# Kernel optimization log

Measured on AMD Instinct MI355X. Metric: run time of the kernel, lower is better.

Reference implementation:

```python
import jax, jax.numpy as jnp
import numpy as np

IN_CH = 32
OUT_CH = 32
M1, M2 = 32, 32
BS, H, W = 8, 256, 256


def setup_inputs() -> dict:
    key = jax.random.key(0)
    kx, kk = jax.random.split(key)
    x = jax.random.normal(kx, (BS, IN_CH, H, W), dtype=jnp.float32)
    # reset_parameters: randn * (1/(in_ch*out_ch)) + 1
    scale = 1.0 / (IN_CH * OUT_CH)
    kernel = jax.random.normal(kk, (2, 1, OUT_CH, M1, M2, 2), dtype=jnp.float32) * scale + 1.0
    r = jnp.float32(1.0)
    return {"x": x, "kernel": kernel, "r": r}


def reference(x, kernel, r):
    # view_as_complex: last dim of 2 -> complex, shape [2, 1, C, M1, M2]
    kc = (kernel[..., 0] + 1j * kernel[..., 1]).astype(jnp.complex64)
    # elementwise complex power kernel**r
    kc = jnp.power(kc, r)

    # forward 2D real FFT over spatial dims (ortho norm)
    x_ft = jnp.fft.rfftn(x, axes=(-2, -1), norm="ortho")  # [bs, C, H, W//2+1]
    Hf, Wr = x_ft.shape[-2], x_ft.shape[-1]
    n1 = min(Hf // 2, M1)
    n2 = min(Wr, M2)

    def mix(block, k):
        # fft over channel dim (-3), multiply by complex kernel, ifft back
        b = jnp.fft.fft(block, axis=-3, norm="ortho")
        b = b * k[..., :n1, :n2]
        return jnp.fft.ifft(b, axis=-3, norm="ortho")

    pos = mix(x_ft[..., :n1, :n2], kc[0])          # low positive freqs
    neg = mix(x_ft[..., Hf - n1:, :n2], kc[1])     # low negative freqs

    out_ft = jnp.zeros((x.shape[0], OUT_CH, Hf, Wr), dtype=jnp.complex64)
    out_ft = out_ft.at[..., :n1, :n2].set(pos)
    out_ft = out_ft.at[..., Hf - n1:, :n2].set(neg)

    # inverse real FFT back to spatial domain
    return jnp.fft.irfftn(out_ft, s=(x.shape[-2], x.shape[-1]), axes=(-2, -1), norm="ortho")
```

## Files before the change

### kernel.cpp

```cpp
#include <hip/hip_runtime.h>
#include <math.h>


#define TWO_PI 6.28318530717958647692f

__global__ __launch_bounds__(256) void kP(const float* __restrict__ kin,
                                          const float* __restrict__ rp,
                                          float2* __restrict__ kp) {
  const int i = blockIdx.x * 256 + threadIdx.x;
  const float r = rp[0];
  const float kr = kin[2 * i], ki = kin[2 * i + 1];
  const float m2 = fmaf(kr, kr, ki * ki);
  float2 o = make_float2(0.f, 0.f);
  if (m2 > 0.f) {
    const float lm = 0.5f * logf(m2);
    const float ang = atan2f(ki, kr);
    const float mag = expf(r * lm);
    float s, c;
    sincosf(r * ang, &s, &c);
    o = make_float2(mag * c, mag * s);
  }
  kp[i] = o;
}

__global__ __launch_bounds__(256) void kA(const float* __restrict__ x,
                                          float2* __restrict__ z1) {
  __shared__ float xs[8192];
  const int tid = threadIdx.x;
  const long row0 = (long)blockIdx.x * 32;
  const float* xg = x + row0 * 256;
  {
    const int xl = tid & 31, rq = tid >> 5;
    const float* xgr = xg + rq * 4 * 256 + xl;
#pragma unroll
    for (int cb = 0; cb < 8; ++cb) {
      const int xc = xl + 32 * cb;
      const float4 v = make_float4(xgr[32 * cb], xgr[32 * cb + 256],
                                   xgr[32 * cb + 512], xgr[32 * cb + 768]);
      *(float4*)(xs + xc * 32 + 4 * ((rq + xc) & 7)) = v;
    }
  }
  __syncthreads();
  for (int i = tid; i < 127 * 32; i += 256) {
    const int xi = 1 + (i >> 5), r = i & 31;
    const int ai = (xi << 5) + ((r + 4 * xi) & 31);
    const int bi = ((256 - xi) << 5) + ((r - 4 * xi) & 31);
    const float a = xs[ai], b = xs[bi];
    xs[ai] = a + b;
    xs[bi] = a - b;
  }
  __syncthreads();
  const int w = tid & 31;
  const int r0 = (tid >> 5) << 2;
  int uo[8];
#pragma unroll
  for (int j = 0; j < 8; ++j) uo[j] = ((r0 + 4 * j) & 31) << 2;
  const float sgn = (w & 1) ? -1.f : 1.f;
  const float4 x0 = *(const float4*)(xs + r0);
  const float4 x128 = *(const float4*)(xs + (128 << 5) + r0);
  float Cr0 = fmaf(sgn, x128.x, x0.x), Cr1 = fmaf(sgn, x128.y, x0.y);
  float Cr2 = fmaf(sgn, x128.z, x0.z), Cr3 = fmaf(sgn, x128.w, x0.w);
  float Ci0 = 0, Ci1 = 0, Ci2 = 0, Ci3 = 0;
  float s1, c1;
  sincosf(TWO_PI * (float)w / 256.0f, &s1, &c1);
  float pc = c1, ps = s1;
  const char* const xsb = (const char*)xs;
#define KA_BODY(UPTR, VPTR)                                        \
  {                                                                \
    const float4 u = *(const float4*)(UPTR);                       \
    const float4 v = *(const float4*)(VPTR);                       \
    Cr0 = fmaf(u.x, pc, Cr0); Ci0 = fmaf(-v.x, ps, Ci0);           \
    Cr1 = fmaf(u.y, pc, Cr1); Ci1 = fmaf(-v.y, ps, Ci1);           \
    Cr2 = fmaf(u.z, pc, Cr2); Ci2 = fmaf(-v.z, ps, Ci2);           \
    Cr3 = fmaf(u.w, pc, Cr3); Ci3 = fmaf(-v.w, ps, Ci3);           \
    const float tn = fmaf(pc, c1, -ps * s1);                       \
    ps = fmaf(pc, s1, ps * c1);                                    \
    pc = tn;                                                       \
  }
  {
    const char* ub = xsb;
    const char* vb = xsb + 249 * 128;
#pragma unroll
    for (int j = 1; j < 8; ++j)
      KA_BODY(ub + j * 128 + uo[j], vb + (7 - j) * 128 + uo[8 - j])
  }
  for (int xb = 8; xb <= 120; xb += 8) {
    const char* ub = xsb + xb * 128;
    const char* vb = xsb + (249 - xb) * 128;
#pragma unroll
    for (int j = 0; j < 8; ++j)
      KA_BODY(ub + j * 128 + uo[j], vb + (7 - j) * 128 + uo[(8 - j) & 7])
  }
#undef KA_BODY
  float2* o = z1 + (row0 + r0) * 32 + w;
  o[0]  = make_float2(Cr0, Ci0);
  o[32] = make_float2(Cr1, Ci1);
  o[64] = make_float2(Cr2, Ci2);
  o[96] = make_float2(Cr3, Ci3);
}

__global__ __launch_bounds__(256) void kB1(float2* __restrict__ z1) {
  const int gt = blockIdx.x * 256 + threadIdx.x;
  const int w = gt & 31, y1 = (gt >> 5) & 31, bc = gt >> 10;
  float2* base = z1 + (long)bc * 8192 + y1 * 32 + w;
  float2 a[8];
#pragma unroll
  for (int j = 0; j < 8; ++j) a[j] = base[j * 1024];
  float2 t0 = make_float2(a[0].x + a[4].x, a[0].y + a[4].y);
  float2 t1 = make_float2(a[0].x - a[4].x, a[0].y - a[4].y);
  float2 t2 = make_float2(a[2].x + a[6].x, a[2].y + a[6].y);
  float2 t3 = make_float2(a[2].x - a[6].x, a[2].y - a[6].y);
  const float2 E0 = make_float2(t0.x + t2.x, t0.y + t2.y);
  const float2 E2 = make_float2(t0.x - t2.x, t0.y - t2.y);
  const float2 E1 = make_float2(t1.x + t3.y, t1.y - t3.x);
  const float2 E3 = make_float2(t1.x - t3.y, t1.y + t3.x);
  t0 = make_float2(a[1].x + a[5].x, a[1].y + a[5].y);
  t1 = make_float2(a[1].x - a[5].x, a[1].y - a[5].y);
  t2 = make_float2(a[3].x + a[7].x, a[3].y + a[7].y);
  t3 = make_float2(a[3].x - a[7].x, a[3].y - a[7].y);
  const float2 O0 = make_float2(t0.x + t2.x, t0.y + t2.y);
  const float2 O2 = make_float2(t0.x - t2.x, t0.y - t2.y);
  const float2 O1 = make_float2(t1.x + t3.y, t1.y - t3.x);
  const float2 O3 = make_float2(t1.x - t3.y, t1.y + t3.x);
  const float RT = 0.70710678118654752440f;
  const float2 B0 = O0;
  const float2 B1 = make_float2(RT * (O1.x + O1.y), RT * (O1.y - O1.x));
  const float2 B2 = make_float2(O2.y, -O2.x);
  const float2 B3 = make_float2(RT * (O3.y - O3.x), -RT * (O3.x + O3.y));
  base[0]        = make_float2(E0.x + B0.x, E0.y + B0.y);
  base[1 * 1024] = make_float2(E1.x + B1.x, E1.y + B1.y);
  base[2 * 1024] = make_float2(E2.x + B2.x, E2.y + B2.y);
  base[3 * 1024] = make_float2(E3.x + B3.x, E3.y + B3.y);
  base[4 * 1024] = make_float2(E0.x - B0.x, E0.y - B0.y);
  base[5 * 1024] = make_float2(E1.x - B1.x, E1.y - B1.y);
  base[6 * 1024] = make_float2(E2.x - B2.x, E2.y - B2.y);
  base[7 * 1024] = make_float2(E3.x - B3.x, E3.y - B3.y);
}

__global__ __launch_bounds__(256) void kB2(const float2* __restrict__ s,
                                           float2* __restrict__ z2) {
  const int bc = blockIdx.x >> 3, tq = blockIdx.x & 7;
  const int k = threadIdx.x >> 5, w = threadIdx.x & 31;
  const int t = tq * 8 + k;
  const int h = (t < 32) ? t : (192 + t);
  float sr, cr;
  sincosf(-TWO_PI * (float)h / 256.0f, &sr, &cr);
  const float2* src = s + (long)bc * 8192 + k * 1024 + w;
  float ar = 0.f, ai = 0.f;
  float pc = 1.f, ps = 0.f;
  for (int y1 = 0; y1 < 32; ++y1) {
    const float2 v = src[y1 * 32];
    ar = fmaf(v.x, pc, fmaf(-v.y, ps, ar));
    ai = fmaf(v.x, ps, fmaf( v.y, pc, ai));
    const float tn = fmaf(pc, cr, -ps * sr);
    ps = fmaf(pc, sr, ps * cr);
    pc = tn;
  }
  z2[(long)bc * 2048 + t * 32 + w] = make_float2(ar, ai);
}

__global__ __launch_bounds__(256) void kC(const float2* __restrict__ z2,
                                          const float2* __restrict__ kp,
                                          float2* __restrict__ g) {
  __shared__ float2 z2s[16 * 33];
  __shared__ float2 fk[16 * 33];
  __shared__ float2 tw[32];
  const int tid = threadIdx.x;
  if (tid < 32) {
    float s, c;
    sincosf(-TWO_PI * (float)tid / 32.0f, &s, &c);
    tw[tid] = make_float2(c, s);
  }
  const int m0 = blockIdx.x * 16;
  const int b = m0 >> 11;
  const int twi = m0 & 2047;
  const int t = twi >> 5;
  const int w0 = twi & 31;
  const int s_ = t >> 5, tm = t & 31;
  for (int i = tid; i < 512; i += 256) {
    const int ci = i >> 4, wj = i & 15;
    const long idx = ((long)(b * 32 + ci)) * 2048 + t * 32 + w0 + wj;
    z2s[wj * 33 + ci] = z2[idx];
  }
  __syncthreads();
  const int m = tid & 15;
  const int p = tid >> 4;
  const int cf0 = 2 * p, cf1 = 2 * p + 1;
  {
    float f0r = 0, f0i = 0, f1r = 0, f1i = 0;
    int i0 = 0, i1 = 0;
#pragma unroll 8
    for (int ci = 0; ci < 32; ++ci) {
      const float2 z = z2s[m * 33 + ci];
      const float2 t0 = tw[i0]; i0 = (i0 + cf0) & 31;
      const float2 t1 = tw[i1]; i1 = (i1 + cf1) & 31;
      f0r = fmaf(z.x, t0.x, fmaf(-z.y, t0.y, f0r));
      f0i = fmaf(z.x, t0.y, fmaf( z.y, t0.x, f0i));
      f1r = fmaf(z.x, t1.x, fmaf(-z.y, t1.y, f1r));
      f1i = fmaf(z.x, t1.y, fmaf( z.y, t1.x, f1i));
    }
    const float2 k0 = kp[((s_ * 32 + cf0) * 32 + tm) * 32 + w0 + m];
    const float2 k1 = kp[((s_ * 32 + cf1) * 32 + tm) * 32 + w0 + m];
    fk[m * 33 + cf0] = make_float2(f0r * k0.x - f0i * k0.y, f0r * k0.y + f0i * k0.x);
    fk[m * 33 + cf1] = make_float2(f1r * k1.x - f1i * k1.y, f1r * k1.y + f1i * k1.x);
  }
  __syncthreads();
  {
    float g0r = 0, g0i = 0, g1r = 0, g1i = 0;
    int i0 = 0, i1 = 0;
    const int co0 = 2 * p, co1 = 2 * p + 1;
#pragma unroll 8
    for (int cf = 0; cf < 32; ++cf) {
      const float2 f = fk[m * 33 + cf];
      const float2 t0 = tw[i0]; i0 = (i0 + co0) & 31;
      const float2 t1 = tw[i1]; i1 = (i1 + co1) & 31;
      g0r = fmaf(f.x, t0.x, fmaf( f.y, t0.y, g0r));
      g0i = fmaf(f.y, t0.x, fmaf(-f.x, t0.y, g0i));
      g1r = fmaf(f.x, t1.x, fmaf( f.y, t1.y, g1r));
      g1i = fmaf(f.y, t1.x, fmaf(-f.x, t1.y, g1i));
    }
    const float SC = 1.0f / 8192.0f;
    g[((long)(b * 32 + co0)) * 2048 + t * 32 + w0 + m] = make_float2(g0r * SC, g0i * SC);
    g[((long)(b * 32 + co1)) * 2048 + t * 32 + w0 + m] = make_float2(g1r * SC, g1i * SC);
  }
}

__global__ __launch_bounds__(256) void kD1(const float2* __restrict__ g,
                                           float2* __restrict__ U) {
  const int bc = blockIdx.x >> 3, y1q = blockIdx.x & 7;
  const int p = threadIdx.x >> 5, w = threadIdx.x & 31;
  const float2* gb = g + (long)bc * 2048 + w;
  float2* ub = U + (long)bc * 8192 + p * 32 + w;
#pragma unroll
  for (int y1l = 0; y1l < 4; ++y1l) {
    const int y1 = y1q * 4 + y1l;
    float st, ct;
    sincosf(TWO_PI * (float)y1 / 32.0f, &st, &ct);
    float s1, c1;
    sincosf(TWO_PI * (float)((p * y1) & 255) / 256.0f, &s1, &c1);
    float s2, c2;
    sincosf(TWO_PI * (float)(((224 + p) * y1) & 255) / 256.0f, &s2, &c2);
    float ar = 0.f, ai = 0.f;
    float pc = c1, ps = s1, qc = c2, qs = s2;
#pragma unroll
    for (int j = 0; j < 4; ++j) {
      const float2 va = gb[(p + 8 * j) * 32];
      const float2 vb = gb[(32 + p + 8 * j) * 32];
      ar = fmaf(va.x, pc, fmaf(-va.y, ps, ar));
      ai = fmaf(va.x, ps, fmaf( va.y, pc, ai));
      ar = fmaf(vb.x, qc, fmaf(-vb.y, qs, ar));
      ai = fmaf(vb.x, qs, fmaf( vb.y, qc, ai));
      const float tn = fmaf(pc, ct, -ps * st);
      ps = fmaf(pc, st, ps * ct);
      pc = tn;
      const float tm = fmaf(qc, ct, -qs * st);
      qs = fmaf(qc, st, qs * ct);
      qc = tm;
    }
    ub[y1 * 256] = make_float2(ar, ai);
  }
}

__global__ __launch_bounds__(256) void kDE(const float2* __restrict__ U,
                                           float* __restrict__ out) {
  __shared__ float2 tst[32 * 34];
  const int tid = threadIdx.x;
  const int bc = blockIdx.x >> 3, yq = blockIdx.x & 7;
  {
    const int y5 = tid >> 3, wq = tid & 7;
    const float* ub = (const float*)(U + (long)bc * 8192 + (long)y5 * 256 + wq * 4);
    float Tr[4] = {0.f, 0.f, 0.f, 0.f}, Ti[4] = {0.f, 0.f, 0.f, 0.f};
#pragma unroll
    for (int p = 0; p < 8; ++p) {
      float sp, cp;
      sincosf(TWO_PI * (float)((p * yq) & 7) / 8.0f, &sp, &cp);
      const float4 qa = *(const float4*)(ub + p * 64);
      const float4 qb = *(const float4*)(ub + p * 64 + 4);
      Tr[0] = fmaf(qa.x, cp, fmaf(-qa.y, sp, Tr[0]));
      Ti[0] = fmaf(qa.x, sp, fmaf( qa.y, cp, Ti[0]));
      Tr[1] = fmaf(qa.z, cp, fmaf(-qa.w, sp, Tr[1]));
      Ti[1] = fmaf(qa.z, sp, fmaf( qa.w, cp, Ti[1]));
      Tr[2] = fmaf(qb.x, cp, fmaf(-qb.y, sp, Tr[2]));
      Ti[2] = fmaf(qb.x, sp, fmaf( qb.y, cp, Ti[2]));
      Tr[3] = fmaf(qb.z, cp, fmaf(-qb.w, sp, Tr[3]));
      Ti[3] = fmaf(qb.z, sp, fmaf( qb.w, cp, Ti[3]));
    }
#pragma unroll
    for (int kk = 0; kk < 4; ++kk) {
      const int w = wq * 4 + kk;
      const float sc = w ? (2.0f / 256.0f) : (1.0f / 256.0f);
      tst[w * 34 + y5] = make_float2(Tr[kk] * sc, Ti[kk] * sc);
    }
  }
  __syncthreads();
  {
    const int xq = tid & 31;
    const int rh = tid >> 5;
    float sb, cb;
    sincosf(TWO_PI * (float)xq / 256.0f, &sb, &cb);
    const float RT = 0.70710678118654752440f;
    const float stc1 = RT * (cb - sb), sts1 = RT * (cb + sb);
    const float stc[4] = {cb, stc1, -sb, -sts1};
    const float sts[4] = {sb, sts1, cb, stc1};
    float C[4][4], S[4][4];
#pragma unroll
    for (int m = 0; m < 4; ++m)
#pragma unroll
      for (int j = 0; j < 4; ++j) { C[m][j] = 0.f; S[m][j] = 0.f; }
    float pc[4] = {1.f, 1.f, 1.f, 1.f}, ps[4] = {0.f, 0.f, 0.f, 0.f};
    const float* tbse = (const float*)tst + rh * 8;
#pragma unroll 2
    for (int w = 0; w < 32; ++w) {
      const float4 q0 = *(const float4*)(tbse + w * 68);
      const float4 q1 = *(const float4*)(tbse + w * 68 + 4);
#pragma unroll
      for (int m = 0; m < 4; ++m) {
        C[m][0] = fmaf(q0.x, pc[m], C[m][0]);
        S[m][0] = fmaf(q0.y, ps[m], S[m][0]);
        C[m][1] = fmaf(q0.z, pc[m], C[m][1]);
        S[m][1] = fmaf(q0.w, ps[m], S[m][1]);
        C[m][2] = fmaf(q1.x, pc[m], C[m][2]);
        S[m][2] = fmaf(q1.y, ps[m], S[m][2]);
        C[m][3] = fmaf(q1.z, pc[m], C[m][3]);
        S[m][3] = fmaf(q1.w, ps[m], S[m][3]);
        const float tn = fmaf(pc[m], stc[m], -ps[m] * sts[m]);
        ps[m] = fmaf(pc[m], sts[m], ps[m] * stc[m]);
        pc[m] = tn;
      }
    }
    const long rbase = (long)bc * 256 + yq * 32;
#pragma unroll
    for (int m = 0; m < 4; ++m) {
      const int xx = xq + 32 * m;
#pragma unroll
      for (int j = 0; j < 4; ++j) {
        const long row = rbase + rh * 4 + j;
        out[row * 256 + xx] = C[m][j] - S[m][j];
        out[row * 256 + ((256 - xx) & 255)] = C[m][j] + S[m][j];
      }
    }
    if (tid < 32) {
      float ae = 0.f, ao = 0.f;
#pragma unroll
      for (int k = 0; k < 16; ++k) {
        ae += tst[(2 * k) * 34 + tid].x;
        ao += tst[(2 * k + 1) * 34 + tid].x;
      }
      out[(rbase + tid) * 256 + 128] = ae - ao;
    }
  }
}

extern "C" void kernel_launch(void* const* d_in, const int* in_sizes, int n_in,
                              void* d_out, int out_size, void* d_ws, size_t ws_size,
                              hipStream_t stream) {
  const float* x = (const float*)d_in[0];
  const float* kin = (const float*)d_in[1];
  const float* rp = (const float*)d_in[2];
  float* out = (float*)d_out;
  char* ws = (char*)d_ws;

  float2* z1 = (float2*)(ws);
  float2* z2 = (float2*)(ws + (16ull << 20));
  float2* kp = (float2*)(ws + (24ull << 20));
  float2* g  = (float2*)(ws);
  float2* U  = (float2*)(ws + (4ull << 20));

  kP<<<256, 256, 0, stream>>>(kin, rp, kp);
  kA<<<2048, 256, 0, stream>>>(x, z1);
  kB1<<<1024, 256, 0, stream>>>(z1);
  kB2<<<2048, 256, 0, stream>>>(z1, z2);
  kC<<<1024, 256, 0, stream>>>(z2, kp, g);
  kD1<<<2048, 256, 0, stream>>>(g, U);
  kDE<<<2048, 256, 0, stream>>>(U, out);
}
```

Before: 217.0 us.

## Replace kA real-DFT folding with radix-8 butterfly and halve kC tile per block

```diff
diff --git a/kernel.cpp b/kernel.cpp
--- a/kernel.cpp
+++ b/kernel.cpp
@@ -41,57 +41,73 @@
     }
   }
   __syncthreads();
-  for (int i = tid; i < 127 * 32; i += 256) {
-    const int xi = 1 + (i >> 5), r = i & 31;
-    const int ai = (xi << 5) + ((r + 4 * xi) & 31);
-    const int bi = ((256 - xi) << 5) + ((r - 4 * xi) & 31);
-    const float a = xs[ai], b = xs[bi];
-    xs[ai] = a + b;
-    xs[bi] = a - b;
+  const float RT = 0.70710678118654752440f;
+#pragma unroll
+  for (int k = 0; k < 4; ++k) {
+    const int i = tid + (k << 8);
+    const int x1 = i >> 5, r = i & 31;
+    float* base = xs + x1 * 32 + ((r + 4 * x1) & 31);
+    const float a0 = base[0],        a1 = base[1024],     a2 = base[2048];
+    const float a3 = base[3 * 1024], a4 = base[4 * 1024], a5 = base[5 * 1024];
+    const float a6 = base[6 * 1024], a7 = base[7 * 1024];
+    const float t0 = a0 + a4, t1 = a0 - a4, t2 = a2 + a6, t3 = a2 - a6;
+    const float u0 = a1 + a5, u1 = a1 - a5, u2 = a3 + a7, u3 = a3 - a7;
+    const float E0 = t0 + t2, O0 = u0 + u2;
+    const float d1 = RT * (u1 - u3), d2 = RT * (u1 + u3);
+    base[0]        = E0 + O0;
+    base[1024]     = E0 - O0;
+    base[2 * 1024] = t1 + d1;
+    base[3 * 1024] = -(t3 + d2);
+    base[4 * 1024] = t0 - t2;
+    base[5 * 1024] = -(u0 - u2);
+    base[6 * 1024] = t1 - d1;
+    base[7 * 1024] = t3 - d2;
   }
   __syncthreads();
   const int w = tid & 31;
   const int r0 = (tid >> 5) << 2;
-  int uo[8];
-#pragma unroll
-  for (int j = 0; j < 8; ++j) uo[j] = ((r0 + 4 * j) & 31) << 2;
-  const float sgn = (w & 1) ? -1.f : 1.f;
-  const float4 x0 = *(const float4*)(xs + r0);
-  const float4 x128 = *(const float4*)(xs + (128 << 5) + r0);
-  float Cr0 = fmaf(sgn, x128.x, x0.x), Cr1 = fmaf(sgn, x128.y, x0.y);
-  float Cr2 = fmaf(sgn, x128.z, x0.z), Cr3 = fmaf(sgn, x128.w, x0.w);
+  const int p = w & 7;
+  int pr, pi;
+  float si;
+  if (p == 0)      { pr = 0;           pi = 0;      si = 0.f; }
+  else if (p == 4) { pr = 1;           pi = 1;      si = 0.f; }
+  else if (p < 4)  { pr = 2 * p;       pi = pr + 1; si = 1.f; }
+  else             { pr = 2 * (8 - p); pi = pr + 1; si = -1.f; }
+  const char* ur = (const char*)xs + pr * 4096;
+  const char* ui = (const char*)xs + pi * 4096;
+  const char* urp[8];
+  const char* uip[8];
+#pragma unroll
+  for (int j = 0; j < 8; ++j) {
+    const int off = 4 * ((r0 + 4 * j) & 31) + 128 * j;
+    urp[j] = ur + off;
+    uip[j] = ui + off;
+  }
+  float s1, c1;
+  sincosf(-TWO_PI * (float)w / 256.0f, &s1, &c1);
+  float pc = 1.f, ps = 0.f;
+  float Cr0 = 0, Cr1 = 0, Cr2 = 0, Cr3 = 0;
   float Ci0 = 0, Ci1 = 0, Ci2 = 0, Ci3 = 0;
-  float s1, c1;
-  sincosf(TWO_PI * (float)w / 256.0f, &s1, &c1);
-  float pc = c1, ps = s1;
-  const char* const xsb = (const char*)xs;
-#define KA_BODY(UPTR, VPTR)                                        \
-  {                                                                \
-    const float4 u = *(const float4*)(UPTR);                       \
-    const float4 v = *(const float4*)(VPTR);                       \
-    Cr0 = fmaf(u.x, pc, Cr0); Ci0 = fmaf(-v.x, ps, Ci0);           \
-    Cr1 = fmaf(u.y, pc, Cr1); Ci1 = fmaf(-v.y, ps, Ci1);           \
-    Cr2 = fmaf(u.z, pc, Cr2); Ci2 = fmaf(-v.z, ps, Ci2);           \
-    Cr3 = fmaf(u.w, pc, Cr3); Ci3 = fmaf(-v.w, ps, Ci3);           \
-    const float tn = fmaf(pc, c1, -ps * s1);                       \
-    ps = fmaf(pc, s1, ps * c1);                                    \
-    pc = tn;                                                       \
-  }
-  {
-    const char* ub = xsb;
-    const char* vb = xsb + 249 * 128;
-#pragma unroll
-    for (int j = 1; j < 8; ++j)
-      KA_BODY(ub + j * 128 + uo[j], vb + (7 - j) * 128 + uo[8 - j])
-  }
-  for (int xb = 8; xb <= 120; xb += 8) {
-    const char* ub = xsb + xb * 128;
-    const char* vb = xsb + (249 - xb) * 128;
-#pragma unroll
-    for (int j = 0; j < 8; ++j)
-      KA_BODY(ub + j * 128 + uo[j], vb + (7 - j) * 128 + uo[(8 - j) & 7])
-  }
-#undef KA_BODY
+#pragma unroll
+  for (int bq = 0; bq < 4; ++bq) {
+#pragma unroll
+    for (int j = 0; j < 8; ++j) {
+      const float4 Fr = *(const float4*)(urp[j] + bq * 1024);
+      const float4 Fi = *(const float4*)(uip[j] + bq * 1024);
+      const float qs = si * ps, qc = si * pc;
+      Cr0 = fmaf(Fr.x, pc, fmaf(-Fi.x, qs, Cr0));
+      Ci0 = fmaf(Fr.x, ps, fmaf( Fi.x, qc, Ci0));
+      Cr1 = fmaf(Fr.y, pc, fmaf(-Fi.y, qs, Cr1));
+      Ci1 = fmaf(Fr.y, ps, fmaf( Fi.y, qc, Ci1));
+      Cr2 = fmaf(Fr.z, pc, fmaf(-Fi.z, qs, Cr2));
+      Ci2 = fmaf(Fr.z, ps, fmaf( Fi.z, qc, Ci2));
+      Cr3 = fmaf(Fr.w, pc, fmaf(-Fi.w, qs, Cr3));
+      Ci3 = fmaf(Fr.w, ps, fmaf( Fi.w, qc, Ci3));
+      const float tn = fmaf(pc, c1, -ps * s1);
+      ps = fmaf(pc, s1, ps * c1);
+      pc = tn;
+    }
+  }
   float2* o = z1 + (row0 + r0) * 32 + w;
   o[0]  = make_float2(Cr0, Ci0);
   o[32] = make_float2(Cr1, Ci1);
@@ -162,8 +178,8 @@
 __global__ __launch_bounds__(256) void kC(const float2* __restrict__ z2,
                                           const float2* __restrict__ kp,
                                           float2* __restrict__ g) {
-  __shared__ float2 z2s[16 * 33];
-  __shared__ float2 fk[16 * 33];
+  __shared__ float2 z2s[8 * 33];
+  __shared__ float2 fk[8 * 33];
   __shared__ float2 tw[32];
   const int tid = threadIdx.x;
   if (tid < 32) {
@@ -171,57 +187,46 @@
     sincosf(-TWO_PI * (float)tid / 32.0f, &s, &c);
     tw[tid] = make_float2(c, s);
   }
-  const int m0 = blockIdx.x * 16;
+  const int m0 = blockIdx.x * 8;
   const int b = m0 >> 11;
   const int twi = m0 & 2047;
   const int t = twi >> 5;
   const int w0 = twi & 31;
   const int s_ = t >> 5, tm = t & 31;
-  for (int i = tid; i < 512; i += 256) {
-    const int ci = i >> 4, wj = i & 15;
-    const long idx = ((long)(b * 32 + ci)) * 2048 + t * 32 + w0 + wj;
-    z2s[wj * 33 + ci] = z2[idx];
-  }
-  __syncthreads();
-  const int m = tid & 15;
-  const int p = tid >> 4;
-  const int cf0 = 2 * p, cf1 = 2 * p + 1;
-  {
-    float f0r = 0, f0i = 0, f1r = 0, f1i = 0;
-    int i0 = 0, i1 = 0;
+  {
+    const int ci = tid >> 3, wj = tid & 7;
+    z2s[wj * 33 + ci] = z2[((long)(b * 32 + ci)) * 2048 + t * 32 + w0 + wj];
+  }
+  __syncthreads();
+  const int m = tid & 7;
+  {
+    const int cf = tid >> 3;
+    float fr = 0, fi = 0;
+    int i0 = 0;
 #pragma unroll 8
     for (int ci = 0; ci < 32; ++ci) {
       const float2 z = z2s[m * 33 + ci];
-      const float2 t0 = tw[i0]; i0 = (i0 + cf0) & 31;
-      const float2 t1 = tw[i1]; i1 = (i1 + cf1) & 31;
-      f0r = fmaf(z.x, t0.x, fmaf(-z.y, t0.y, f0r));
-      f0i = fmaf(z.x, t0.y, fmaf( z.y, t0.x, f0i));
-      f1r = fmaf(z.x, t1.x, fmaf(-z.y, t1.y, f1r));
-      f1i = fmaf(z.x, t1.y, fmaf( z.y, t1.x, f1i));
-    }
-    const float2 k0 = kp[((s_ * 32 + cf0) * 32 + tm) * 32 + w0 + m];
-    const float2 k1 = kp[((s_ * 32 + cf1) * 32 + tm) * 32 + w0 + m];
-    fk[m * 33 + cf0] = make_float2(f0r * k0.x - f0i * k0.y, f0r * k0.y + f0i * k0.x);
-    fk[m * 33 + cf1] = make_float2(f1r * k1.x - f1i * k1.y, f1r * k1.y + f1i * k1.x);
-  }
-  __syncthreads();
-  {
-    float g0r = 0, g0i = 0, g1r = 0, g1i = 0;
-    int i0 = 0, i1 = 0;
-    const int co0 = 2 * p, co1 = 2 * p + 1;
+      const float2 t0 = tw[i0]; i0 = (i0 + cf) & 31;
+      fr = fmaf(z.x, t0.x, fmaf(-z.y, t0.y, fr));
+      fi = fmaf(z.x, t0.y, fmaf( z.y, t0.x, fi));
+    }
+    const float2 k0 = kp[((s_ * 32 + cf) * 32 + tm) * 32 + w0 + m];
+    fk[m * 33 + cf] = make_float2(fr * k0.x - fi * k0.y, fr * k0.y + fi * k0.x);
+  }
+  __syncthreads();
+  {
+    const int co = tid >> 3;
+    float gr = 0, gi = 0;
+    int i0 = 0;
 #pragma unroll 8
     for (int cf = 0; cf < 32; ++cf) {
       const float2 f = fk[m * 33 + cf];
-      const float2 t0 = tw[i0]; i0 = (i0 + co0) & 31;
-      const float2 t1 = tw[i1]; i1 = (i1 + co1) & 31;
-      g0r = fmaf(f.x, t0.x, fmaf( f.y, t0.y, g0r));
-      g0i = fmaf(f.y, t0.x, fmaf(-f.x, t0.y, g0i));
-      g1r = fmaf(f.x, t1.x, fmaf( f.y, t1.y, g1r));
-      g1i = fmaf(f.y, t1.x, fmaf(-f.x, t1.y, g1i));
+      const float2 t0 = tw[i0]; i0 = (i0 + co) & 31;
+      gr = fmaf(f.x, t0.x, fmaf( f.y, t0.y, gr));
+      gi = fmaf(f.y, t0.x, fmaf(-f.x, t0.y, gi));
     }
     const float SC = 1.0f / 8192.0f;
-    g[((long)(b * 32 + co0)) * 2048 + t * 32 + w0 + m] = make_float2(g0r * SC, g0i * SC);
-    g[((long)(b * 32 + co1)) * 2048 + t * 32 + w0 + m] = make_float2(g1r * SC, g1i * SC);
+    g[((long)(b * 32 + co)) * 2048 + t * 32 + w0 + m] = make_float2(gr * SC, gi * SC);
   }
 }
 
@@ -253,9 +258,9 @@
       const float tn = fmaf(pc, ct, -ps * st);
       ps = fmaf(pc, st, ps * ct);
       pc = tn;
-      const float tm = fmaf(qc, ct, -qs * st);
+      const float tm2 = fmaf(qc, ct, -qs * st);
       qs = fmaf(qc, st, qs * ct);
-      qc = tm;
+      qc = tm2;
     }
     ub[y1 * 256] = make_float2(ar, ai);
   }
@@ -370,7 +375,7 @@
   kA<<<2048, 256, 0, stream>>>(x, z1);
   kB1<<<1024, 256, 0, stream>>>(z1);
   kB2<<<2048, 256, 0, stream>>>(z1, z2);
-  kC<<<1024, 256, 0, stream>>>(z2, kp, g);
+  kC<<<2048, 256, 0, stream>>>(z2, kp, g);
   kD1<<<2048, 256, 0, stream>>>(g, U);
   kDE<<<2048, 256, 0, stream>>>(U, out);
 }
```

After: 202.9 us. 1.07x faster.
